# Kernel tuning notes

Hardware: AMD Instinct MI355X
Metric: run time of the kernel (lower is better)

Reference implementation:

```python
import jax, jax.numpy as jnp
import numpy as np

HEADS = 8
EPS = 1e-5


def setup_inputs() -> dict:
    key = jax.random.key(0)
    B, N, C = 32, 4096, 256
    headc = C // HEADS
    x = jax.random.normal(key, (B, N, C), dtype=jnp.float32)
    return {
        "x": x,
        "kln_weight": jnp.ones((HEADS, 1, headc), dtype=jnp.float32),
        "kln_bias": jnp.zeros((HEADS, 1, headc), dtype=jnp.float32),
        "vln_weight": jnp.ones((HEADS, 1, headc), dtype=jnp.float32),
        "vln_bias": jnp.zeros((HEADS, 1, headc), dtype=jnp.float32),
    }


def _ln(t, w, b, headc):
    # Faithful to the torch module: unbiased std (ddof=1), eps added to std (not var).
    m = jnp.mean(t, axis=-1, keepdims=True)
    d = t - m
    std = jnp.sqrt(jnp.sum(d * d, axis=-1, keepdims=True) / (headc - 1))
    return w * (d / (std + EPS)) + b


def reference(x, kln_weight, kln_bias, vln_weight, vln_bias):
    B, N, C = x.shape
    headc = C // HEADS
    # [B, H, N, D]
    qkv = x.reshape(B, N, HEADS, headc).transpose(0, 2, 1, 3)
    k = _ln(qkv, kln_weight, kln_bias, headc)
    v = _ln(qkv, vln_weight, vln_bias, headc)
    # k^T v : [B, H, D, D], scaled by 1/N
    kv = jnp.einsum("bhnd,bhne->bhde", k, v) / N
    # q (k^T v): [B, H, N, D]
    out = jnp.einsum("bhnd,bhde->bhne", qkv, kv)
    out = out.transpose(0, 2, 1, 3).reshape(B, N, C)
    return out + x
```

## Files before the change

### kernel.cpp

```cpp
#include <hip/hip_runtime.h>

#define H_ 8
#define D_ 32
#define B_ 32
#define N_ 4096
#define C_ 256
#define EPS_ 1e-5f

typedef __attribute__((ext_vector_type(8))) short bf16x8;
typedef __attribute__((ext_vector_type(4))) float f32x4;

__device__ __forceinline__ short f2bf(float f) {
    unsigned u = __builtin_bit_cast(unsigned, f);
    unsigned r = (u + 0x7FFFu + ((u >> 16) & 1u)) >> 16;
    return (short)r;
}

__device__ __forceinline__ int uidx(int r, int c) {
    return r * 40 + ((r >> 3) & 3) * 16 + c;
}

__global__ __launch_bounds__(256, 4)
void k1_skv(const float* __restrict__ x, float* __restrict__ Sws, float* __restrict__ Tws)
{
    __shared__ short ubuf[256 * 40 + 64];

    const int tid  = threadIdx.x;
    const int bh   = blockIdx.x >> 2;
    const int q4   = blockIdx.x & 3;
    const int b    = bh >> 3;
    const int h    = bh & 7;
    const int lane = tid & 63;
    const int wave = tid >> 6;
    const int g    = lane >> 4;
    const int cL   = lane & 15;

    f32x4 acc[2][2] = {};
    f32x4 tq[2] = {};

    bf16x8 ones;
    #pragma unroll
    for (int j = 0; j < 8; ++j) ones[j] = (short)0x3F80;

    const float* xbase = x + ((size_t)b * N_ + q4 * 1024) * C_ + h * D_;

    float4 xr[8];
    {
        const float4* p = reinterpret_cast<const float4*>(xbase + (size_t)tid * C_);
        #pragma unroll
        for (int c = 0; c < 8; ++c) xr[c] = p[c];
    }

    for (int it = 0; it < 4; ++it) {
        float sum = 0.f, sq = 0.f;
        #pragma unroll
        for (int c = 0; c < 8; ++c) {
            const float4 a = xr[c];
            sum += a.x + a.y + a.z + a.w;
            sq = fmaf(a.x, a.x, fmaf(a.y, a.y, fmaf(a.z, a.z, fmaf(a.w, a.w, sq))));
        }
        const float m   = sum * (1.f / 32.f);
        const float ss  = fmaxf(sq - sum * m, 0.f);
        const float inv = 1.f / (sqrtf(ss * (1.f / 31.f)) + EPS_);

        bf16x8 wv[4];
        #pragma unroll
        for (int q = 0; q < 4; ++q) {
            const float4 a0 = xr[q * 2 + 0];
            const float4 a1 = xr[q * 2 + 1];
            wv[q][0] = f2bf((a0.x - m) * inv); wv[q][1] = f2bf((a0.y - m) * inv);
            wv[q][2] = f2bf((a0.z - m) * inv); wv[q][3] = f2bf((a0.w - m) * inv);
            wv[q][4] = f2bf((a1.x - m) * inv); wv[q][5] = f2bf((a1.y - m) * inv);
            wv[q][6] = f2bf((a1.z - m) * inv); wv[q][7] = f2bf((a1.w - m) * inv);
        }

        __syncthreads();
        {
            const int base = tid * 40 + ((tid >> 3) & 3) * 16;
            #pragma unroll
            for (int q = 0; q < 4; ++q)
                *reinterpret_cast<bf16x8*>(&ubuf[base + q * 8]) = wv[q];
        }
        __syncthreads();

        if (it < 3) {
            const float4* p = reinterpret_cast<const float4*>(
                xbase + ((size_t)(it + 1) * 256 + tid) * C_);
            #pragma unroll
            for (int c = 0; c < 8; ++c) xr[c] = p[c];
        }

        #pragma unroll
        for (int ks = 0; ks < 2; ++ks) {
            const int R0 = wave * 64 + ks * 32 + 8 * g;
            bf16x8 F0, F1;
            #pragma unroll
            for (int j = 0; j < 8; ++j) {
                const int base = uidx(R0 + j, cL);
                F0[j] = ubuf[base];
                F1[j] = ubuf[base + 16];
            }
            tq[0] = __builtin_amdgcn_mfma_f32_16x16x32_bf16(ones, F0, tq[0], 0, 0, 0);
            tq[1] = __builtin_amdgcn_mfma_f32_16x16x32_bf16(ones, F1, tq[1], 0, 0, 0);
            acc[0][0] = __builtin_amdgcn_mfma_f32_16x16x32_bf16(F0, F0, acc[0][0], 0, 0, 0);
            acc[0][1] = __builtin_amdgcn_mfma_f32_16x16x32_bf16(F0, F1, acc[0][1], 0, 0, 0);
            acc[1][0] = __builtin_amdgcn_mfma_f32_16x16x32_bf16(F1, F0, acc[1][0], 0, 0, 0);
            acc[1][1] = __builtin_amdgcn_mfma_f32_16x16x32_bf16(F1, F1, acc[1][1], 0, 0, 0);
        }
    }

    float* Sb = Sws + (size_t)bh * (D_ * D_);
    const int mr = g * 4;
    #pragma unroll
    for (int ca = 0; ca < 2; ++ca)
        #pragma unroll
        for (int cb = 0; cb < 2; ++cb)
            #pragma unroll
            for (int r = 0; r < 4; ++r)
                atomicAdd(Sb + (ca * 16 + mr + r) * D_ + cb * 16 + cL, acc[ca][cb][r]);

    if (lane < 16) {
        atomicAdd(Tws + bh * D_ + cL,      tq[0][0]);
        atomicAdd(Tws + bh * D_ + 16 + cL, tq[1][0]);
    }
}

__global__ __launch_bounds__(256, 4)
void k2_out(const float* __restrict__ x,
            const float* __restrict__ Sws, const float* __restrict__ Tws,
            const float* __restrict__ kw, const float* __restrict__ kb,
            const float* __restrict__ vw, const float* __restrict__ vb,
            float* __restrict__ out)
{
    __shared__ float xbuf[4 * C_];

    const int tid   = threadIdx.x;
    const int b     = blockIdx.x >> 6;
    const int chunk = blockIdx.x & 63;
    const int h     = tid >> 5;
    const int e     = tid & 31;
    const int bh    = b * 8 + h;

    const float* S = Sws + (size_t)bh * (D_ * D_);
    const float* T = Tws + bh * D_;
    const float wve  = vw[h * D_ + e];
    const float bve  = vb[h * D_ + e];
    const float Te   = T[e];
    const float invN = 1.f / (float)N_;

    float kvc[32];
    #pragma unroll
    for (int d = 0; d < D_; ++d) {
        const float wkd = kw[h * D_ + d];
        const float bkd = kb[h * D_ + d];
        kvc[d] = invN * (wkd * (wve * S[d * D_ + e] + bve * T[d]) + bkd * wve * Te)
               + bkd * bve;
    }

    for (int it = 0; it < 16; ++it) {
        const int r0 = chunk * 64 + it * 4;
        const float* xrow = x + ((size_t)b * N_ + r0) * C_;
        const float4 xv = reinterpret_cast<const float4*>(xrow)[tid];
        __syncthreads();
        reinterpret_cast<float4*>(xbuf)[tid] = xv;
        __syncthreads();

        float res[4];
        #pragma unroll
        for (int r = 0; r < 4; ++r) {
            const float4* xr4 = reinterpret_cast<const float4*>(xbuf + r * C_ + h * D_);
            float dot = 0.f;
            #pragma unroll
            for (int c = 0; c < 8; ++c) {
                const float4 a = xr4[c];
                dot += a.x * kvc[c * 4 + 0] + a.y * kvc[c * 4 + 1]
                     + a.z * kvc[c * 4 + 2] + a.w * kvc[c * 4 + 3];
            }
            res[r] = dot + xbuf[r * C_ + tid];
        }
        float* orow = out + ((size_t)b * N_ + r0) * C_;
        #pragma unroll
        for (int r = 0; r < 4; ++r) orow[r * C_ + tid] = res[r];
    }
}

extern "C" void kernel_launch(void* const* d_in, const int* in_sizes, int n_in,
                              void* d_out, int out_size, void* d_ws, size_t ws_size,
                              hipStream_t stream)
{
    const float* x  = (const float*)d_in[0];
    const float* kw = (const float*)d_in[1];
    const float* kb = (const float*)d_in[2];
    const float* vw = (const float*)d_in[3];
    const float* vb = (const float*)d_in[4];
    float* outp = (float*)d_out;

    float* Sws = (float*)d_ws;
    float* Tws = Sws + (size_t)B_ * H_ * D_ * D_;
    const size_t zero_bytes =
        ((size_t)B_ * H_ * D_ * D_ + (size_t)B_ * H_ * D_) * sizeof(float);
    hipMemsetAsync(d_ws, 0, zero_bytes, stream);

    k1_skv<<<dim3(B_ * H_ * 4), dim3(256), 0, stream>>>(x, Sws, Tws);
    k2_out<<<dim3(B_ * 64), dim3(256), 0, stream>>>(x, Sws, Tws, kw, kb, vw, vb, outp);
}
```

Measured before the change: 100.5 us.

## Split k1 over 8 row chunks, use 8-thread rows and block-reduce S before atomics

```diff
diff --git a/kernel.cpp b/kernel.cpp
--- a/kernel.cpp
+++ b/kernel.cpp
@@ -8,6 +8,7 @@
 #define EPS_ 1e-5f
 
 typedef __attribute__((ext_vector_type(8))) short bf16x8;
+typedef __attribute__((ext_vector_type(4))) short bf16x4;
 typedef __attribute__((ext_vector_type(4))) float f32x4;
 
 __device__ __forceinline__ short f2bf(float f) {
@@ -20,14 +21,14 @@
     return r * 40 + ((r >> 3) & 3) * 16 + c;
 }
 
-__global__ __launch_bounds__(256, 4)
+__global__ __launch_bounds__(256, 6)
 void k1_skv(const float* __restrict__ x, float* __restrict__ Sws, float* __restrict__ Tws)
 {
-    __shared__ short ubuf[256 * 40 + 64];
+    __shared__ short ubuf[128 * 40 + 56];
 
     const int tid  = threadIdx.x;
-    const int bh   = blockIdx.x >> 2;
-    const int q4   = blockIdx.x & 3;
+    const int bh   = blockIdx.x >> 3;
+    const int q8   = blockIdx.x & 7;
     const int b    = bh >> 3;
     const int h    = bh & 7;
     const int lane = tid & 63;
@@ -35,6 +36,9 @@
     const int g    = lane >> 4;
     const int cL   = lane & 15;
 
+    const int rsub = tid >> 3;
+    const int csub = tid & 7;
+
     f32x4 acc[2][2] = {};
     f32x4 tq[2] = {};
 
@@ -42,57 +46,51 @@
     #pragma unroll
     for (int j = 0; j < 8; ++j) ones[j] = (short)0x3F80;
 
-    const float* xbase = x + ((size_t)b * N_ + q4 * 1024) * C_ + h * D_;
-
-    float4 xr[8];
-    {
-        const float4* p = reinterpret_cast<const float4*>(xbase + (size_t)tid * C_);
-        #pragma unroll
-        for (int c = 0; c < 8; ++c) xr[c] = p[c];
-    }
+    const float* xbase = x + ((size_t)b * N_ + q8 * 512) * C_ + h * D_;
+
+    float4 xr[4];
+    #pragma unroll
+    for (int k = 0; k < 4; ++k)
+        xr[k] = *reinterpret_cast<const float4*>(
+            xbase + (size_t)(k * 32 + rsub) * C_ + csub * 4);
 
     for (int it = 0; it < 4; ++it) {
-        float sum = 0.f, sq = 0.f;
-        #pragma unroll
-        for (int c = 0; c < 8; ++c) {
-            const float4 a = xr[c];
-            sum += a.x + a.y + a.z + a.w;
-            sq = fmaf(a.x, a.x, fmaf(a.y, a.y, fmaf(a.z, a.z, fmaf(a.w, a.w, sq))));
-        }
-        const float m   = sum * (1.f / 32.f);
-        const float ss  = fmaxf(sq - sum * m, 0.f);
-        const float inv = 1.f / (sqrtf(ss * (1.f / 31.f)) + EPS_);
-
-        bf16x8 wv[4];
-        #pragma unroll
-        for (int q = 0; q < 4; ++q) {
-            const float4 a0 = xr[q * 2 + 0];
-            const float4 a1 = xr[q * 2 + 1];
-            wv[q][0] = f2bf((a0.x - m) * inv); wv[q][1] = f2bf((a0.y - m) * inv);
-            wv[q][2] = f2bf((a0.z - m) * inv); wv[q][3] = f2bf((a0.w - m) * inv);
-            wv[q][4] = f2bf((a1.x - m) * inv); wv[q][5] = f2bf((a1.y - m) * inv);
-            wv[q][6] = f2bf((a1.z - m) * inv); wv[q][7] = f2bf((a1.w - m) * inv);
-        }
-
-        __syncthreads();
+        bf16x4 wv[4];
+        #pragma unroll
+        for (int k = 0; k < 4; ++k) {
+            const float4 a = xr[k];
+            float sum = a.x + a.y + a.z + a.w;
+            float sq  = a.x * a.x + a.y * a.y + a.z * a.z + a.w * a.w;
+            #pragma unroll
+            for (int m = 1; m < 8; m <<= 1) {
+                sum += __shfl_xor(sum, m);
+                sq  += __shfl_xor(sq,  m);
+            }
+            const float mean = sum * (1.f / 32.f);
+            const float ss   = fmaxf(sq - sum * mean, 0.f);
+            const float inv  = 1.f / (sqrtf(ss * (1.f / 31.f)) + EPS_);
+            wv[k][0] = f2bf((a.x - mean) * inv);
+            wv[k][1] = f2bf((a.y - mean) * inv);
+            wv[k][2] = f2bf((a.z - mean) * inv);
+            wv[k][3] = f2bf((a.w - mean) * inv);
+        }
+
+        __syncthreads();
+        #pragma unroll
+        for (int k = 0; k < 4; ++k)
+            *reinterpret_cast<bf16x4*>(&ubuf[uidx(k * 32 + rsub, csub * 4)]) = wv[k];
+        __syncthreads();
+
+        if (it < 3) {
+            const float* nb = xbase + (size_t)(it + 1) * 128 * C_;
+            #pragma unroll
+            for (int k = 0; k < 4; ++k)
+                xr[k] = *reinterpret_cast<const float4*>(
+                    nb + (size_t)(k * 32 + rsub) * C_ + csub * 4);
+        }
+
         {
-            const int base = tid * 40 + ((tid >> 3) & 3) * 16;
-            #pragma unroll
-            for (int q = 0; q < 4; ++q)
-                *reinterpret_cast<bf16x8*>(&ubuf[base + q * 8]) = wv[q];
-        }
-        __syncthreads();
-
-        if (it < 3) {
-            const float4* p = reinterpret_cast<const float4*>(
-                xbase + ((size_t)(it + 1) * 256 + tid) * C_);
-            #pragma unroll
-            for (int c = 0; c < 8; ++c) xr[c] = p[c];
-        }
-
-        #pragma unroll
-        for (int ks = 0; ks < 2; ++ks) {
-            const int R0 = wave * 64 + ks * 32 + 8 * g;
+            const int R0 = wave * 32 + 8 * g;
             bf16x8 F0, F1;
             #pragma unroll
             for (int j = 0; j < 8; ++j) {
@@ -109,15 +107,38 @@
         }
     }
 
-    float* Sb = Sws + (size_t)bh * (D_ * D_);
-    const int mr = g * 4;
-    #pragma unroll
-    for (int ca = 0; ca < 2; ++ca)
-        #pragma unroll
-        for (int cb = 0; cb < 2; ++cb)
-            #pragma unroll
-            for (int r = 0; r < 4; ++r)
-                atomicAdd(Sb + (ca * 16 + mr + r) * D_ + cb * 16 + cL, acc[ca][cb][r]);
+    __syncthreads();
+    float* sred = reinterpret_cast<float*>(ubuf);
+    float* dst  = sred + (wave & 1) * 1024;
+    if (wave < 2) {
+        #pragma unroll
+        for (int ca = 0; ca < 2; ++ca)
+            #pragma unroll
+            for (int cb = 0; cb < 2; ++cb)
+                #pragma unroll
+                for (int r = 0; r < 4; ++r)
+                    dst[(ca * 16 + g * 4 + r) * D_ + cb * 16 + cL] = acc[ca][cb][r];
+    }
+    __syncthreads();
+    if (wave >= 2) {
+        #pragma unroll
+        for (int ca = 0; ca < 2; ++ca)
+            #pragma unroll
+            for (int cb = 0; cb < 2; ++cb)
+                #pragma unroll
+                for (int r = 0; r < 4; ++r)
+                    dst[(ca * 16 + g * 4 + r) * D_ + cb * 16 + cL] += acc[ca][cb][r];
+    }
+    __syncthreads();
+    {
+        float* Sb = Sws + (size_t)bh * (D_ * D_);
+        const float4 va = *reinterpret_cast<const float4*>(&sred[tid * 4]);
+        const float4 vb = *reinterpret_cast<const float4*>(&sred[1024 + tid * 4]);
+        atomicAdd(Sb + tid * 4 + 0, va.x + vb.x);
+        atomicAdd(Sb + tid * 4 + 1, va.y + vb.y);
+        atomicAdd(Sb + tid * 4 + 2, va.z + vb.z);
+        atomicAdd(Sb + tid * 4 + 3, va.w + vb.w);
+    }
 
     if (lane < 16) {
         atomicAdd(Tws + bh * D_ + cL,      tq[0][0]);
@@ -201,6 +222,6 @@
         ((size_t)B_ * H_ * D_ * D_ + (size_t)B_ * H_ * D_) * sizeof(float);
     hipMemsetAsync(d_ws, 0, zero_bytes, stream);
 
-    k1_skv<<<dim3(B_ * H_ * 4), dim3(256), 0, stream>>>(x, Sws, Tws);
+    k1_skv<<<dim3(B_ * H_ * 8), dim3(256), 0, stream>>>(x, Sws, Tws);
     k2_out<<<dim3(B_ * 64), dim3(256), 0, stream>>>(x, Sws, Tws, kw, kb, vw, vb, outp);
 }
```

After: 112.8 us. +12.2%, slower.

## Split k1 row range across more blocks and pre-reduce waves in LDS

Applied to the files above, without the earlier changes.

```diff
diff --git a/kernel.cpp b/kernel.cpp
--- a/kernel.cpp
+++ b/kernel.cpp
@@ -26,8 +26,8 @@
     __shared__ short ubuf[256 * 40 + 64];
 
     const int tid  = threadIdx.x;
-    const int bh   = blockIdx.x >> 2;
-    const int q4   = blockIdx.x & 3;
+    const int bh   = blockIdx.x >> 4;
+    const int q16  = blockIdx.x & 15;
     const int b    = bh >> 3;
     const int h    = bh & 7;
     const int lane = tid & 63;
@@ -42,82 +42,89 @@
     #pragma unroll
     for (int j = 0; j < 8; ++j) ones[j] = (short)0x3F80;
 
-    const float* xbase = x + ((size_t)b * N_ + q4 * 1024) * C_ + h * D_;
-
+    const float* xrow = x + ((size_t)b * N_ + q16 * 256 + tid) * C_ + h * D_;
     float4 xr[8];
+    #pragma unroll
+    for (int c = 0; c < 8; ++c)
+        xr[c] = reinterpret_cast<const float4*>(xrow)[c];
+
+    float sum = 0.f, sq = 0.f;
+    #pragma unroll
+    for (int c = 0; c < 8; ++c) {
+        const float4 a = xr[c];
+        sum += a.x + a.y + a.z + a.w;
+        sq = fmaf(a.x, a.x, fmaf(a.y, a.y, fmaf(a.z, a.z, fmaf(a.w, a.w, sq))));
+    }
+    const float m   = sum * (1.f / 32.f);
+    const float ss  = fmaxf(sq - sum * m, 0.f);
+    const float inv = 1.f / (sqrtf(ss * (1.f / 31.f)) + EPS_);
+
     {
-        const float4* p = reinterpret_cast<const float4*>(xbase + (size_t)tid * C_);
-        #pragma unroll
-        for (int c = 0; c < 8; ++c) xr[c] = p[c];
-    }
-
-    for (int it = 0; it < 4; ++it) {
-        float sum = 0.f, sq = 0.f;
-        #pragma unroll
-        for (int c = 0; c < 8; ++c) {
-            const float4 a = xr[c];
-            sum += a.x + a.y + a.z + a.w;
-            sq = fmaf(a.x, a.x, fmaf(a.y, a.y, fmaf(a.z, a.z, fmaf(a.w, a.w, sq))));
-        }
-        const float m   = sum * (1.f / 32.f);
-        const float ss  = fmaxf(sq - sum * m, 0.f);
-        const float inv = 1.f / (sqrtf(ss * (1.f / 31.f)) + EPS_);
-
-        bf16x8 wv[4];
+        const int base = tid * 40 + ((tid >> 3) & 3) * 16;
         #pragma unroll
         for (int q = 0; q < 4; ++q) {
             const float4 a0 = xr[q * 2 + 0];
             const float4 a1 = xr[q * 2 + 1];
-            wv[q][0] = f2bf((a0.x - m) * inv); wv[q][1] = f2bf((a0.y - m) * inv);
-            wv[q][2] = f2bf((a0.z - m) * inv); wv[q][3] = f2bf((a0.w - m) * inv);
-            wv[q][4] = f2bf((a1.x - m) * inv); wv[q][5] = f2bf((a1.y - m) * inv);
-            wv[q][6] = f2bf((a1.z - m) * inv); wv[q][7] = f2bf((a1.w - m) * inv);
+            bf16x8 wv;
+            wv[0] = f2bf((a0.x - m) * inv); wv[1] = f2bf((a0.y - m) * inv);
+            wv[2] = f2bf((a0.z - m) * inv); wv[3] = f2bf((a0.w - m) * inv);
+            wv[4] = f2bf((a1.x - m) * inv); wv[5] = f2bf((a1.y - m) * inv);
+            wv[6] = f2bf((a1.z - m) * inv); wv[7] = f2bf((a1.w - m) * inv);
+            *reinterpret_cast<bf16x8*>(&ubuf[base + q * 8]) = wv;
         }
-
-        __syncthreads();
-        {
-            const int base = tid * 40 + ((tid >> 3) & 3) * 16;
+    }
+    asm volatile("s_waitcnt lgkmcnt(0)" ::: "memory");
+
+    #pragma unroll
+    for (int ks = 0; ks < 2; ++ks) {
+        const int R0 = wave * 64 + ks * 32 + 8 * g;
+        bf16x8 F0, F1;
+        #pragma unroll
+        for (int j = 0; j < 8; ++j) {
+            const int base = uidx(R0 + j, cL);
+            F0[j] = ubuf[base];
+            F1[j] = ubuf[base + 16];
+        }
+        tq[0] = __builtin_amdgcn_mfma_f32_16x16x32_bf16(ones, F0, tq[0], 0, 0, 0);
+        tq[1] = __builtin_amdgcn_mfma_f32_16x16x32_bf16(ones, F1, tq[1], 0, 0, 0);
+        acc[0][0] = __builtin_amdgcn_mfma_f32_16x16x32_bf16(F0, F0, acc[0][0], 0, 0, 0);
+        acc[0][1] = __builtin_amdgcn_mfma_f32_16x16x32_bf16(F0, F1, acc[0][1], 0, 0, 0);
+        acc[1][0] = __builtin_amdgcn_mfma_f32_16x16x32_bf16(F1, F0, acc[1][0], 0, 0, 0);
+        acc[1][1] = __builtin_amdgcn_mfma_f32_16x16x32_bf16(F1, F1, acc[1][1], 0, 0, 0);
+    }
+
+    __syncthreads();
+    float* sred = reinterpret_cast<float*>(ubuf);
+    float* dst  = sred + (wave & 1) * 1024;
+    if (wave < 2) {
+        #pragma unroll
+        for (int ca = 0; ca < 2; ++ca)
             #pragma unroll
-            for (int q = 0; q < 4; ++q)
-                *reinterpret_cast<bf16x8*>(&ubuf[base + q * 8]) = wv[q];
-        }
-        __syncthreads();
-
-        if (it < 3) {
-            const float4* p = reinterpret_cast<const float4*>(
-                xbase + ((size_t)(it + 1) * 256 + tid) * C_);
+            for (int cb = 0; cb < 2; ++cb)
+                #pragma unroll
+                for (int r = 0; r < 4; ++r)
+                    dst[(ca * 16 + g * 4 + r) * D_ + cb * 16 + cL] = acc[ca][cb][r];
+    }
+    __syncthreads();
+    if (wave >= 2) {
+        #pragma unroll
+        for (int ca = 0; ca < 2; ++ca)
             #pragma unroll
-            for (int c = 0; c < 8; ++c) xr[c] = p[c];
-        }
-
-        #pragma unroll
-        for (int ks = 0; ks < 2; ++ks) {
-            const int R0 = wave * 64 + ks * 32 + 8 * g;
-            bf16x8 F0, F1;
-            #pragma unroll
-            for (int j = 0; j < 8; ++j) {
-                const int base = uidx(R0 + j, cL);
-                F0[j] = ubuf[base];
-                F1[j] = ubuf[base + 16];
-            }
-            tq[0] = __builtin_amdgcn_mfma_f32_16x16x32_bf16(ones, F0, tq[0], 0, 0, 0);
-            tq[1] = __builtin_amdgcn_mfma_f32_16x16x32_bf16(ones, F1, tq[1], 0, 0, 0);
-            acc[0][0] = __builtin_amdgcn_mfma_f32_16x16x32_bf16(F0, F0, acc[0][0], 0, 0, 0);
-            acc[0][1] = __builtin_amdgcn_mfma_f32_16x16x32_bf16(F0, F1, acc[0][1], 0, 0, 0);
-            acc[1][0] = __builtin_amdgcn_mfma_f32_16x16x32_bf16(F1, F0, acc[1][0], 0, 0, 0);
-            acc[1][1] = __builtin_amdgcn_mfma_f32_16x16x32_bf16(F1, F1, acc[1][1], 0, 0, 0);
-        }
-    }
-
-    float* Sb = Sws + (size_t)bh * (D_ * D_);
-    const int mr = g * 4;
-    #pragma unroll
-    for (int ca = 0; ca < 2; ++ca)
-        #pragma unroll
-        for (int cb = 0; cb < 2; ++cb)
-            #pragma unroll
-            for (int r = 0; r < 4; ++r)
-                atomicAdd(Sb + (ca * 16 + mr + r) * D_ + cb * 16 + cL, acc[ca][cb][r]);
+            for (int cb = 0; cb < 2; ++cb)
+                #pragma unroll
+                for (int r = 0; r < 4; ++r)
+                    dst[(ca * 16 + g * 4 + r) * D_ + cb * 16 + cL] += acc[ca][cb][r];
+    }
+    __syncthreads();
+    {
+        float* Sb = Sws + (size_t)bh * (D_ * D_);
+        const float4 va = *reinterpret_cast<const float4*>(&sred[tid * 4]);
+        const float4 vb = *reinterpret_cast<const float4*>(&sred[1024 + tid * 4]);
+        atomicAdd(Sb + tid * 4 + 0, va.x + vb.x);
+        atomicAdd(Sb + tid * 4 + 1, va.y + vb.y);
+        atomicAdd(Sb + tid * 4 + 2, va.z + vb.z);
+        atomicAdd(Sb + tid * 4 + 3, va.w + vb.w);
+    }
 
     if (lane < 16) {
         atomicAdd(Tws + bh * D_ + cL,      tq[0][0]);
@@ -201,6 +208,6 @@
         ((size_t)B_ * H_ * D_ * D_ + (size_t)B_ * H_ * D_) * sizeof(float);
     hipMemsetAsync(d_ws, 0, zero_bytes, stream);
 
-    k1_skv<<<dim3(B_ * H_ * 4), dim3(256), 0, stream>>>(x, Sws, Tws);
+    k1_skv<<<dim3(B_ * H_ * 16), dim3(256), 0, stream>>>(x, Sws, Tws);
     k2_out<<<dim3(B_ * 64), dim3(256), 0, stream>>>(x, Sws, Tws, kw, kb, vw, vb, outp);
 }
```

New measurement: 130.7 us. +30.0%, slower.
